# Performance work log

Measured on AMD Instinct MI355X. Metric: run time of the kernel, lower is better.

Reference implementation:

```python
import jax, jax.numpy as jnp
import numpy as np

NC, NU, K, C, P, O = 20, 16, 128, 2048, 5, 256

def setup_inputs() -> dict:
    key = jax.random.key(0)
    ks = jax.random.split(key, 6)
    s = 0.02  # keep activations well-scaled
    return {
        "topk_feats": jax.random.normal(ks[0], (NC, NU, K, C), jnp.float32),
        "prototypes": jax.random.normal(ks[1], (NC, P, C), jnp.float32),
        "w_inner1": jax.random.normal(ks[2], (O, C), jnp.float32) * s,
        "w_inner_trans": jax.random.normal(ks[3], (C, C), jnp.float32) * s,
        "w_inter1": jax.random.normal(ks[4], (O, C), jnp.float32) * s,
        "w_inter2": jax.random.normal(ks[5], (O, C), jnp.float32) * s,
    }

def reference(topk_feats, prototypes, w_inner1, w_inner_trans, w_inter1, w_inter2):
    scale = 1.0 / jnp.sqrt(jnp.asarray(O, topk_feats.dtype))
    # --- inner (per-group) self-attention, vmapped over (class, unlabel) ---
    # fe: [nc, nu, k, o]
    fe = jnp.einsum("nukc,oc->nuko", topk_feats, w_inner1)
    att = jax.nn.softmax(jnp.einsum("nuko,nulo->nukl", fe, fe) * scale, axis=-1)
    agg = jnp.einsum("nukl,nulc->nukc", att, topk_feats)  # atte @ feat
    feats = topk_feats + jax.nn.relu(jnp.einsum("nukc,dc->nukd", agg, w_inner_trans))
    # --- inter (prototype -> all feats) cross-attention per class ---
    fa = feats.reshape(NC, NU * K, C)  # cat over unlabel dim
    fae = jnp.einsum("nmc,oc->nmo", fa, w_inter1)
    pe = jnp.einsum("npc,oc->npo", prototypes, w_inter2)
    att2 = jax.nn.softmax(jnp.einsum("npo,nmo->npm", pe, fae) * scale, axis=-1)
    un_protos = jnp.einsum("npm,nmc->npc", att2, fa)  # [nc, p, c]
    return un_protos
```

## Files before the change

kernel.cpp:

```cpp
#include <hip/hip_runtime.h>

typedef __attribute__((ext_vector_type(4))) float f32x4;
typedef __attribute__((ext_vector_type(8))) short short8;

#define DEVI static __device__ __forceinline__

DEVI unsigned short f2bf(float f) {
  unsigned int u = __float_as_uint(f);
  u += 0x7FFFu + ((u >> 16) & 1u);
  return (unsigned short)(u >> 16);
}
DEVI float bf2f(unsigned short s) { return __uint_as_float(((unsigned int)s) << 16); }
DEVI unsigned int pack2(float lo, float hi) {
  return ((unsigned int)f2bf(hi) << 16) | (unsigned int)f2bf(lo);
}

#define GL2LDS(gp, lp)                                                        \
  __builtin_amdgcn_global_load_lds(                                           \
      (const __attribute__((address_space(1))) void*)(const void*)(gp),       \
      (__attribute__((address_space(3))) void*)(void*)(lp), 16, 0, 0)

#define BARRIER __builtin_amdgcn_s_barrier()
#define LGKM0                                                                 \
  do {                                                                        \
    asm volatile("s_waitcnt lgkmcnt(0)" ::: "memory");                        \
    __builtin_amdgcn_sched_barrier(0);                                        \
  } while (0)

__global__ __launch_bounds__(256) void k_cvt_bf16(const float* __restrict__ src,
                                                  unsigned short* __restrict__ dst, int n4) {
  int i = blockIdx.x * 256 + threadIdx.x;
  if (i < n4) {
    float4 v = ((const float4*)src)[i];
    uint2 o; o.x = pack2(v.x, v.y); o.y = pack2(v.z, v.w);
    ((uint2*)dst)[i] = o;
  }
}

template <bool RES>
__global__ __launch_bounds__(256) void k_gemm_bt(const unsigned short* __restrict__ A,
                                                 const unsigned short* __restrict__ B,
                                                 unsigned short* __restrict__ C,
                                                 const float* __restrict__ resid, int N) {
  constexpr int K = 2048;
  __shared__ unsigned short lA[2][128 * 64];
  __shared__ unsigned short lB[2][128 * 64];
  const int tid = threadIdx.x;
  const int lane = tid & 63;
  const int wave = tid >> 6;
  const int wr = wave >> 1, wc = wave & 1;
  const int nx = gridDim.x;
  const int lin = blockIdx.y * nx + blockIdx.x;
  const int cpx = (nx * gridDim.y) >> 3;
  const int swz = (lin & 7) * cpx + (lin >> 3);
  const long mBase = (long)(swz / nx) * 128;
  const long nBase = (long)(swz % nx) * 128;

  f32x4 acc[4][4] = {};

  auto stage = [&](int buf, int k0) {
#pragma unroll
    for (int it = 0; it < 4; it++) {
      int idx = it * 256 + tid;
      int row = idx >> 3, kc = idx & 7;
      int skc = kc ^ (row & 7);
      int lbase = (it * 256 + (tid & ~63)) * 8;
      GL2LDS(A + (mBase + row) * (long)K + k0 + skc * 8, &lA[buf][lbase]);
      GL2LDS(B + (nBase + row) * (long)K + k0 + skc * 8, &lB[buf][lbase]);
    }
  };

  stage(0, 0);
  for (int t = 0; t < 32; t++) {
    const int cur = t & 1;
    if (t < 31) {
      stage(cur ^ 1, (t + 1) * 64);
      asm volatile("s_waitcnt vmcnt(8)" ::: "memory");
    } else {
      asm volatile("s_waitcnt vmcnt(0)" ::: "memory");
    }
    __builtin_amdgcn_s_barrier();
    __builtin_amdgcn_sched_barrier(0);
    const unsigned short* bA = &lA[cur][0];
    const unsigned short* bB = &lB[cur][0];
#pragma unroll
    for (int kb = 0; kb < 2; kb++) {
      short8 af[4], bfr[4];
#pragma unroll
      for (int mt = 0; mt < 4; mt++) {
        int row = wr * 64 + mt * 16 + (lane & 15);
        int slot = (kb * 4 + (lane >> 4)) ^ (row & 7);
        af[mt] = *(const short8*)&bA[row * 64 + slot * 8];
      }
#pragma unroll
      for (int nt = 0; nt < 4; nt++) {
        int row = wc * 64 + nt * 16 + (lane & 15);
        int slot = (kb * 4 + (lane >> 4)) ^ (row & 7);
        bfr[nt] = *(const short8*)&bB[row * 64 + slot * 8];
      }
#pragma unroll
      for (int mt = 0; mt < 4; mt++)
#pragma unroll
        for (int nt = 0; nt < 4; nt++)
          acc[mt][nt] = __builtin_amdgcn_mfma_f32_16x16x32_bf16(af[mt], bfr[nt], acc[mt][nt], 0, 0, 0);
    }
    __builtin_amdgcn_sched_barrier(0);
    __builtin_amdgcn_s_barrier();
  }
#pragma unroll
  for (int mt = 0; mt < 4; mt++) {
#pragma unroll
    for (int nt = 0; nt < 4; nt++) {
#pragma unroll
      for (int j = 0; j < 4; j++) {
        long row = mBase + wr * 64 + mt * 16 + (lane >> 4) * 4 + j;
        long col = nBase + wc * 64 + nt * 16 + (lane & 15);
        float v = acc[mt][nt][j];
        if constexpr (RES) v = resid[row * (long)N + col] + fmaxf(v, 0.0f);
        C[row * (long)N + col] = f2bf(v);
      }
    }
  }
}

template <bool RES>
__global__ __launch_bounds__(512, 1) void k_gemm256_8p(const unsigned short* __restrict__ A,
                                                       const unsigned short* __restrict__ B,
                                                       unsigned short* __restrict__ C,
                                                       const unsigned short* __restrict__ residb,
                                                       int N) {
  constexpr int K = 2048;
  __shared__ unsigned short lA[2][2][128 * 64];
  __shared__ unsigned short lB[2][2][128 * 64];
  const int tid = threadIdx.x;
  const int lane = tid & 63;
  const int wave = tid >> 6;
  const int wr = wave >> 2, wc = wave & 3;
  const int lin = blockIdx.y * 8 + blockIdx.x;
  const int swz = (lin & 7) * 160 + (lin >> 3);
  const long mBase = (long)(swz >> 3) * 256;
  const long nBase = (long)(swz & 7) * 256;

  f32x4 acc[8][4] = {};
  short8 af[4][2];
  short8 bfr[4][2];

  auto stageA = [&](int buf, int half, int t) {
    const unsigned short* base = A + (mBase + half * 128) * (long)K + (long)t * 64;
    unsigned short* lds = &lA[buf][half][0];
#pragma unroll
    for (int it = 0; it < 2; it++) {
      int r = it * 64 + (tid >> 3);
      int kc = tid & 7;
      int skc = kc ^ (r & 7);
      GL2LDS(base + (long)r * K + skc * 8, lds + (it * 512 + (tid & ~63)) * 8);
    }
  };
  auto stageB = [&](int buf, int half, int t) {
    const unsigned short* base = B + (nBase + half * 128) * (long)K + (long)t * 64;
    unsigned short* lds = &lB[buf][half][0];
#pragma unroll
    for (int it = 0; it < 2; it++) {
      int r = it * 64 + (tid >> 3);
      int kc = tid & 7;
      int skc = kc ^ (r & 7);
      GL2LDS(base + (long)r * K + skc * 8, lds + (it * 512 + (tid & ~63)) * 8);
    }
  };
  auto readA = [&](int buf, int mhalf) {
#pragma unroll
    for (int mt = 0; mt < 4; mt++)
#pragma unroll
      for (int kb = 0; kb < 2; kb++) {
        int r = mhalf * 64 + mt * 16 + (lane & 15);
        int slot = (kb * 4 + (lane >> 4)) ^ (r & 7);
        af[mt][kb] = *(const short8*)&lA[buf][wr][r * 64 + slot * 8];
      }
  };
  auto readB = [&](int buf, int nh) {
#pragma unroll
    for (int ntl = 0; ntl < 2; ntl++)
#pragma unroll
      for (int kb = 0; kb < 2; kb++) {
        int nt = nh * 2 + ntl;
        int col = wc * 64 + nt * 16 + (lane & 15);
        int half = col >> 7, r = col & 127;
        int slot = (kb * 4 + (lane >> 4)) ^ (r & 7);
        bfr[nt][kb] = *(const short8*)&lB[buf][half][r * 64 + slot * 8];
      }
  };
  auto mfmaQ = [&](int mhalf, int nh) {
    __builtin_amdgcn_s_setprio(1);
#pragma unroll
    for (int kb = 0; kb < 2; kb++)
#pragma unroll
      for (int mt = 0; mt < 4; mt++)
#pragma unroll
        for (int ntl = 0; ntl < 2; ntl++) {
          int nt = nh * 2 + ntl;
          acc[mhalf * 4 + mt][nt] = __builtin_amdgcn_mfma_f32_16x16x32_bf16(
              af[mt][kb], bfr[nt][kb], acc[mhalf * 4 + mt][nt], 0, 0, 0);
        }
    __builtin_amdgcn_s_setprio(0);
  };

  stageA(0, 0, 0); stageA(0, 1, 0); stageB(0, 0, 0); stageB(0, 1, 0);
  stageA(1, 0, 1); stageA(1, 1, 1); stageB(1, 0, 1); stageB(1, 1, 1);
  asm volatile("s_waitcnt vmcnt(8)" ::: "memory");
  BARRIER;

  for (int t = 0; t < 32; t++) {
    const int cur = t & 1;
    readA(cur, 0);
    readB(cur, 0);
    if (t >= 1 && t <= 30) stageA(cur ^ 1, 1, t + 1);
    BARRIER; LGKM0;
    mfmaQ(0, 0);
    BARRIER;
    readB(cur, 1);
    BARRIER; LGKM0;
    mfmaQ(0, 1);
    BARRIER;
    readA(cur, 1);
    if (t <= 29) stageB(cur, 0, t + 2);
    BARRIER; LGKM0;
    mfmaQ(1, 0);
    BARRIER;
    if (t <= 29) { stageB(cur, 1, t + 2); stageA(cur, 0, t + 2); }
    mfmaQ(1, 1);
    if (t <= 29) {
      asm volatile("s_waitcnt vmcnt(6)" ::: "memory");
    } else if (t == 30) {
      asm volatile("s_waitcnt vmcnt(0)" ::: "memory");
    }
    BARRIER;
  }

#pragma unroll
  for (int mt = 0; mt < 8; mt++) {
#pragma unroll
    for (int nt = 0; nt < 4; nt++) {
#pragma unroll
      for (int j = 0; j < 4; j++) {
        long row = mBase + wr * 128 + mt * 16 + (lane >> 4) * 4 + j;
        long col = nBase + wc * 64 + nt * 16 + (lane & 15);
        float v = acc[mt][nt][j];
        if constexpr (RES) v = bf2f(residb[row * (long)N + col]) + fmaxf(v, 0.0f);
        C[row * (long)N + col] = f2bf(v);
      }
    }
  }
}

__global__ __launch_bounds__(256) void k_attn_inner(const unsigned short* __restrict__ fe,
                                                    const unsigned short* __restrict__ topkb,
                                                    unsigned short* __restrict__ agg) {
  __shared__ unsigned short attb[128 * 136];
  __shared__ unsigned short featT[64 * 128];
  __shared__ float redmax[2 * 128];
  __shared__ float redsum[2 * 128];
  const int tid = threadIdx.x;
  const int lane = tid & 63;
  const int wave = tid >> 6;
  const int wr = wave >> 1, wc = wave & 1;
  const int g = blockIdx.x;
  const unsigned short* feG = fe + (long)g * 128 * 256;

  f32x4 s[4][4] = {};
#pragma unroll
  for (int kb = 0; kb < 8; kb++) {
    short8 af[4], bfr[4];
#pragma unroll
    for (int mt = 0; mt < 4; mt++) {
      int row = wr * 64 + mt * 16 + (lane & 15);
      af[mt] = *(const short8*)(feG + row * 256 + kb * 32 + (lane >> 4) * 8);
    }
#pragma unroll
    for (int nt = 0; nt < 4; nt++) {
      int row = wc * 64 + nt * 16 + (lane & 15);
      bfr[nt] = *(const short8*)(feG + row * 256 + kb * 32 + (lane >> 4) * 8);
    }
#pragma unroll
    for (int mt = 0; mt < 4; mt++)
#pragma unroll
      for (int nt = 0; nt < 4; nt++)
        s[mt][nt] = __builtin_amdgcn_mfma_f32_16x16x32_bf16(af[mt], bfr[nt], s[mt][nt], 0, 0, 0);
  }

  const float cexp = 0.0625f * 1.44269504088896f;
#pragma unroll
  for (int mt = 0; mt < 4; mt++) {
#pragma unroll
    for (int j = 0; j < 4; j++) {
      float m = fmaxf(fmaxf(s[mt][0][j], s[mt][1][j]), fmaxf(s[mt][2][j], s[mt][3][j]));
#pragma unroll
      for (int d = 1; d < 16; d <<= 1) m = fmaxf(m, __shfl_xor(m, d, 64));
      int r = wr * 64 + mt * 16 + (lane >> 4) * 4 + j;
      if ((lane & 15) == 0) redmax[wc * 128 + r] = m;
    }
  }
  __syncthreads();
#pragma unroll
  for (int mt = 0; mt < 4; mt++) {
#pragma unroll
    for (int j = 0; j < 4; j++) {
      int r = wr * 64 + mt * 16 + (lane >> 4) * 4 + j;
      float M = fmaxf(redmax[r], redmax[128 + r]);
      float sm = 0.f;
#pragma unroll
      for (int nt = 0; nt < 4; nt++) {
        float p = exp2f((s[mt][nt][j] - M) * cexp);
        s[mt][nt][j] = p;
        sm += p;
      }
#pragma unroll
      for (int d = 1; d < 16; d <<= 1) sm += __shfl_xor(sm, d, 64);
      if ((lane & 15) == 0) redsum[wc * 128 + r] = sm;
    }
  }
  __syncthreads();
#pragma unroll
  for (int mt = 0; mt < 4; mt++) {
#pragma unroll
    for (int j = 0; j < 4; j++) {
      int r = wr * 64 + mt * 16 + (lane >> 4) * 4 + j;
      float inv = 1.0f / (redsum[r] + redsum[128 + r]);
#pragma unroll
      for (int nt = 0; nt < 4; nt++) {
        int c = wc * 64 + nt * 16 + (lane & 15);
        attb[r * 136 + c] = f2bf(s[mt][nt][j] * inv);
      }
    }
  }

  for (int ch = 0; ch < 32; ch++) {
    __syncthreads();
#pragma unroll
    for (int i = 0; i < 4; i++) {
      int seg = i * 256 + tid;
      int l = seg >> 3, kc = seg & 7;
      const unsigned short* gp = topkb + ((long)g * 128 + l) * 2048 + ch * 64 + kc * 8;
      uint4 w = *(const uint4*)gp;
      unsigned short v[8];
      v[0] = (unsigned short)(w.x & 0xffff); v[1] = (unsigned short)(w.x >> 16);
      v[2] = (unsigned short)(w.y & 0xffff); v[3] = (unsigned short)(w.y >> 16);
      v[4] = (unsigned short)(w.z & 0xffff); v[5] = (unsigned short)(w.z >> 16);
      v[6] = (unsigned short)(w.w & 0xffff); v[7] = (unsigned short)(w.w >> 16);
      int lx = l ^ (kc << 3);
#pragma unroll
      for (int j = 0; j < 8; j++) featT[(kc * 8 + j) * 128 + lx] = v[j];
    }
    __syncthreads();
    f32x4 c[2][4] = {};
#pragma unroll
    for (int kb = 0; kb < 4; kb++) {
      short8 af2[2], bf2v[4];
#pragma unroll
      for (int mt = 0; mt < 2; mt++) {
        int r = wave * 32 + mt * 16 + (lane & 15);
        af2[mt] = *(const short8*)&attb[r * 136 + kb * 32 + (lane >> 4) * 8];
      }
#pragma unroll
      for (int nt = 0; nt < 4; nt++) {
        int cc = nt * 16 + (lane & 15);
        int l0 = (kb * 32 + (lane >> 4) * 8) ^ (((cc >> 3) & 7) << 3);
        bf2v[nt] = *(const short8*)&featT[cc * 128 + l0];
      }
#pragma unroll
      for (int mt = 0; mt < 2; mt++)
#pragma unroll
        for (int nt = 0; nt < 4; nt++)
          c[mt][nt] = __builtin_amdgcn_mfma_f32_16x16x32_bf16(af2[mt], bf2v[nt], c[mt][nt], 0, 0, 0);
    }
#pragma unroll
    for (int mt = 0; mt < 2; mt++)
#pragma unroll
      for (int nt = 0; nt < 4; nt++)
#pragma unroll
        for (int j = 0; j < 4; j++) {
          long row = (long)g * 128 + wave * 32 + mt * 16 + (lane >> 4) * 4 + j;
          int col = ch * 64 + nt * 16 + (lane & 15);
          agg[row * 2048 + col] = f2bf(c[mt][nt][j]);
        }
  }
}

__global__ __launch_bounds__(256) void k_pe(const float* __restrict__ protos,
                                            const float* __restrict__ wi2,
                                            float* __restrict__ pe) {
  int n = blockIdx.x, oc = blockIdx.y, tid = threadIdx.x;
  if (tid < 160) {
    int p = tid >> 5, o = oc * 32 + (tid & 31);
    const float* pr = protos + ((long)n * 5 + p) * 2048;
    const float* wr = wi2 + (long)o * 2048;
    float acc = 0.f;
    for (int cidx = 0; cidx < 2048; cidx += 4) {
      float4 a = *(const float4*)(pr + cidx);
      float4 b = *(const float4*)(wr + cidx);
      acc += a.x * b.x + a.y * b.y + a.z * b.z + a.w * b.w;
    }
    pe[((long)n * 5 + p) * 256 + o] = acc;
  }
}

__global__ __launch_bounds__(256) void k_q(const float* __restrict__ pe,
                                           const float* __restrict__ wi1,
                                           float* __restrict__ q) {
  __shared__ float pel[1280];
  int n = blockIdx.x, cb = blockIdx.y, tid = threadIdx.x;
  for (int i = tid; i < 1280; i += 256) pel[i] = pe[(long)n * 1280 + i];
  __syncthreads();
  int c = cb * 256 + tid;
  float a[5] = {0.f, 0.f, 0.f, 0.f, 0.f};
  for (int o = 0; o < 256; o++) {
    float w = wi1[(long)o * 2048 + c];
#pragma unroll
    for (int p = 0; p < 5; p++) a[p] += pel[p * 256 + o] * w;
  }
#pragma unroll
  for (int p = 0; p < 5; p++) q[((long)n * 5 + p) * 2048 + c] = a[p];
}

__global__ __launch_bounds__(256) void k_lg(const float* __restrict__ q,
                                            const unsigned short* __restrict__ feats,
                                            float* __restrict__ lgp) {
  __shared__ float ql[5 * 1024];
  int n = blockIdx.x, mc = blockIdx.y, cb = blockIdx.z, tid = threadIdx.x;
  const float4* qs = (const float4*)(q + (long)n * 5 * 2048);
  for (int i = tid; i < 1280; i += 256) {
    int p = i >> 8, r = i & 255;
    ((float4*)ql)[i] = qs[p * 512 + cb * 256 + r];
  }
  __syncthreads();
  int m = mc * 256 + tid;
  const unsigned short* fr = feats + ((long)n * 2048 + m) * 2048 + cb * 1024;
  float a[5] = {0.f, 0.f, 0.f, 0.f, 0.f};
  for (int c = 0; c < 1024; c += 8) {
    uint4 w = *(const uint4*)(fr + c);
    float f[8];
    f[0] = bf2f((unsigned short)(w.x & 0xffff)); f[1] = bf2f((unsigned short)(w.x >> 16));
    f[2] = bf2f((unsigned short)(w.y & 0xffff)); f[3] = bf2f((unsigned short)(w.y >> 16));
    f[4] = bf2f((unsigned short)(w.z & 0xffff)); f[5] = bf2f((unsigned short)(w.z >> 16));
    f[6] = bf2f((unsigned short)(w.w & 0xffff)); f[7] = bf2f((unsigned short)(w.w >> 16));
#pragma unroll
    for (int j = 0; j < 8; j++) {
      float fv = f[j];
#pragma unroll
      for (int p = 0; p < 5; p++) a[p] += fv * ql[p * 1024 + c + j];
    }
  }
#pragma unroll
  for (int p = 0; p < 5; p++)
    lgp[((long)cb * 100 + n * 5 + p) * 2048 + m] = a[p] * 0.0625f;
}

__global__ __launch_bounds__(256) void k_sm(const float* __restrict__ lgp,
                                            float* __restrict__ att2) {
  __shared__ float red[4], red2[4];
  int b = blockIdx.x, tid = threadIdx.x;
  const float* s0 = lgp + (long)b * 2048;
  const float* s1 = lgp + (long)100 * 2048 + (long)b * 2048;
  float v[8];
  float mx = -1e30f;
#pragma unroll
  for (int i = 0; i < 8; i++) {
    v[i] = s0[i * 256 + tid] + s1[i * 256 + tid];
    mx = fmaxf(mx, v[i]);
  }
#pragma unroll
  for (int d = 1; d < 64; d <<= 1) mx = fmaxf(mx, __shfl_xor(mx, d, 64));
  if ((tid & 63) == 0) red[tid >> 6] = mx;
  __syncthreads();
  mx = fmaxf(fmaxf(red[0], red[1]), fmaxf(red[2], red[3]));
  float sm = 0.f;
#pragma unroll
  for (int i = 0; i < 8; i++) { v[i] = exp2f((v[i] - mx) * 1.44269504088896f); sm += v[i]; }
#pragma unroll
  for (int d = 1; d < 64; d <<= 1) sm += __shfl_xor(sm, d, 64);
  if ((tid & 63) == 0) red2[tid >> 6] = sm;
  __syncthreads();
  float inv = 1.0f / (red2[0] + red2[1] + red2[2] + red2[3]);
  float* dst = att2 + (long)b * 2048;
#pragma unroll
  for (int i = 0; i < 8; i++) dst[i * 256 + tid] = v[i] * inv;
}

__global__ __launch_bounds__(256) void k_out_part(const float* __restrict__ att2,
                                                  const unsigned short* __restrict__ feats,
                                                  float* __restrict__ partial) {
  __shared__ float a2[5 * 512];
  int n = blockIdx.x, cb = blockIdx.y, ms = blockIdx.z;
  int tid = threadIdx.x;
  const float* src = att2 + (long)n * 5 * 2048 + ms * 512;
  for (int i = tid; i < 640; i += 256) {
    int p = i >> 7, qq = i & 127;
    ((float4*)a2)[i] = *(const float4*)(src + p * 2048 + qq * 4);
  }
  __syncthreads();
  int c0 = cb * 512 + tid * 2;
  const unsigned short* fp = feats + ((long)n * 2048 + ms * 512) * 2048 + c0;
  float acc[5][2] = {};
  for (int m = 0; m < 512; m++) {
    unsigned int w = *(const unsigned int*)(fp + (long)m * 2048);
    float f0 = bf2f((unsigned short)(w & 0xffff));
    float f1 = bf2f((unsigned short)(w >> 16));
#pragma unroll
    for (int p = 0; p < 5; p++) {
      float a = a2[p * 512 + m];
      acc[p][0] += a * f0;
      acc[p][1] += a * f1;
    }
  }
  float* pp = partial + ((long)ms * 100 + (long)n * 5) * 2048;
#pragma unroll
  for (int p = 0; p < 5; p++) {
    float2 o; o.x = acc[p][0]; o.y = acc[p][1];
    *(float2*)(pp + p * 2048 + c0) = o;
  }
}

__global__ __launch_bounds__(256) void k_out_red(const float* __restrict__ partial,
                                                 float* __restrict__ outp) {
  int i = blockIdx.x * 256 + threadIdx.x;
  const f32x4* P = (const f32x4*)partial;
  f32x4 s = P[i] + P[51200 + i] + P[2 * 51200 + i] + P[3 * 51200 + i];
  ((f32x4*)outp)[i] = s;
}

extern "C" void kernel_launch(void* const* d_in, const int* in_sizes, int n_in,
                              void* d_out, int out_size, void* d_ws, size_t ws_size,
                              hipStream_t stream) {
  const float* topk = (const float*)d_in[0];
  const float* protos = (const float*)d_in[1];
  const float* w1 = (const float*)d_in[2];
  const float* wt = (const float*)d_in[3];
  const float* wi1 = (const float*)d_in[4];
  const float* wi2 = (const float*)d_in[5];
  float* outp = (float*)d_out;

  char* ws = (char*)d_ws;
  size_t off = 0;
  auto alloc = [&](size_t bytes) -> void* {
    void* p = ws + off;
    off += (bytes + 255) & ~(size_t)255;
    return p;
  };
  unsigned short* w1b = (unsigned short*)alloc((size_t)256 * 2048 * 2);
  unsigned short* wtb = (unsigned short*)alloc((size_t)2048 * 2048 * 2);
  unsigned short* topkb = (unsigned short*)alloc((size_t)40960 * 2048 * 2);
  unsigned short* fe = (unsigned short*)alloc((size_t)40960 * 256 * 2);
  unsigned short* agg = (unsigned short*)alloc((size_t)40960 * 2048 * 2);
  float* pe = (float*)alloc((size_t)20 * 5 * 256 * 4);
  float* q = (float*)alloc((size_t)20 * 5 * 2048 * 4);
  float* lgp = (float*)alloc((size_t)2 * 100 * 2048 * 4);
  float* att2 = (float*)alloc((size_t)20 * 5 * 2048 * 4);
  float* partial = (float*)alloc((size_t)4 * 100 * 2048 * 4);
  unsigned short* feats = topkb;

  k_cvt_bf16<<<512, 256, 0, stream>>>(w1, w1b, 131072);
  k_cvt_bf16<<<4096, 256, 0, stream>>>(wt, wtb, 1048576);
  k_cvt_bf16<<<81920, 256, 0, stream>>>(topk, topkb, 20971520);

  k_gemm_bt<false><<<dim3(2, 320), 256, 0, stream>>>(topkb, w1b, fe, nullptr, 256);
  k_attn_inner<<<320, 256, 0, stream>>>(fe, topkb, agg);
  k_gemm256_8p<true><<<dim3(8, 160), 512, 0, stream>>>(agg, wtb, feats, topkb, 2048);
  k_pe<<<dim3(20, 8), 256, 0, stream>>>(protos, wi2, pe);
  k_q<<<dim3(20, 8), 256, 0, stream>>>(pe, wi1, q);
  k_lg<<<dim3(20, 8, 2), 256, 0, stream>>>(q, feats, lgp);
  k_sm<<<100, 256, 0, stream>>>(lgp, att2);
  k_out_part<<<dim3(20, 4, 4), 256, 0, stream>>>(att2, feats, partial);
  k_out_red<<<200, 256, 0, stream>>>(partial, outp);
}
```

Measured before the change: 898.8 us.

## Fuse topk fp32-to-bf16 conversion into the fe GEMM and split inter-attention kernels wider

The fp32 top-k features are now read directly by a new fe GEMM kernel. It converts them to bf16 in registers, writes the bf16 copy to global memory for later stages, and feeds them to MFMA through LDS. The w1 operand is loaded straight from global into registers. This removes the separate large conversion pass and one re-read of the bf16 features. The k_lg and k_out_part kernels split the reduction over 8 chunks instead of 2 or 4, which raises grid parallelism at the cost of more partial buffers to reduce.

```diff
diff --git a/kernel.cpp b/kernel.cpp
--- a/kernel.cpp
+++ b/kernel.cpp
@@ -37,90 +37,104 @@
   }
 }
 
-template <bool RES>
-__global__ __launch_bounds__(256) void k_gemm_bt(const unsigned short* __restrict__ A,
-                                                 const unsigned short* __restrict__ B,
-                                                 unsigned short* __restrict__ C,
-                                                 const float* __restrict__ resid, int N) {
-  constexpr int K = 2048;
-  __shared__ unsigned short lA[2][128 * 64];
-  __shared__ unsigned short lB[2][128 * 64];
+__global__ __launch_bounds__(512, 1) void k_fe(const float* __restrict__ topk,
+                                               const unsigned short* __restrict__ w1b,
+                                               unsigned short* __restrict__ topkb,
+                                               unsigned short* __restrict__ fe) {
+  __shared__ unsigned short lA[128 * 64];
   const int tid = threadIdx.x;
   const int lane = tid & 63;
   const int wave = tid >> 6;
-  const int wr = wave >> 1, wc = wave & 1;
-  const int nx = gridDim.x;
-  const int lin = blockIdx.y * nx + blockIdx.x;
-  const int cpx = (nx * gridDim.y) >> 3;
-  const int swz = (lin & 7) * cpx + (lin >> 3);
-  const long mBase = (long)(swz / nx) * 128;
-  const long nBase = (long)(swz % nx) * 128;
+  const int wr = wave >> 2, wc = wave & 3;
+  const long mBase = (long)blockIdx.x * 128;
+
+  const int arow = tid >> 2;
+  const int aq = tid & 3;
+  const float* aptr = topk + (mBase + arow) * 2048 + aq * 16;
 
   f32x4 acc[4][4] = {};
-
-  auto stage = [&](int buf, int k0) {
-#pragma unroll
-    for (int it = 0; it < 4; it++) {
-      int idx = it * 256 + tid;
-      int row = idx >> 3, kc = idx & 7;
-      int skc = kc ^ (row & 7);
-      int lbase = (it * 256 + (tid & ~63)) * 8;
-      GL2LDS(A + (mBase + row) * (long)K + k0 + skc * 8, &lA[buf][lbase]);
-      GL2LDS(B + (nBase + row) * (long)K + k0 + skc * 8, &lB[buf][lbase]);
-    }
-  };
-
-  stage(0, 0);
+  float4 a4[2][4];
+  short8 bfv[2][4][2];
+
+  auto loadB = [&](int buf, int t) {
+#pragma unroll
+    for (int nt = 0; nt < 4; nt++)
+#pragma unroll
+      for (int kb = 0; kb < 2; kb++) {
+        int o = wc * 64 + nt * 16 + (lane & 15);
+        bfv[buf][nt][kb] =
+            *(const short8*)(w1b + (long)o * 2048 + t * 64 + kb * 32 + (lane >> 4) * 8);
+      }
+  };
+  auto loadA = [&](int buf, int t) {
+#pragma unroll
+    for (int i = 0; i < 4; i++) a4[buf][i] = *(const float4*)(aptr + t * 64 + i * 4);
+  };
+
+  loadB(0, 0);
+  loadA(0, 0);
+
   for (int t = 0; t < 32; t++) {
     const int cur = t & 1;
     if (t < 31) {
-      stage(cur ^ 1, (t + 1) * 64);
-      asm volatile("s_waitcnt vmcnt(8)" ::: "memory");
+      loadB(cur ^ 1, t + 1);
+      loadA(cur ^ 1, t + 1);
+      asm volatile("s_waitcnt vmcnt(12)" ::: "memory");
     } else {
       asm volatile("s_waitcnt vmcnt(0)" ::: "memory");
     }
-    __builtin_amdgcn_s_barrier();
     __builtin_amdgcn_sched_barrier(0);
-    const unsigned short* bA = &lA[cur][0];
-    const unsigned short* bB = &lB[cur][0];
-#pragma unroll
-    for (int kb = 0; kb < 2; kb++) {
-      short8 af[4], bfr[4];
-#pragma unroll
-      for (int mt = 0; mt < 4; mt++) {
-        int row = wr * 64 + mt * 16 + (lane & 15);
-        int slot = (kb * 4 + (lane >> 4)) ^ (row & 7);
-        af[mt] = *(const short8*)&bA[row * 64 + slot * 8];
-      }
-#pragma unroll
-      for (int nt = 0; nt < 4; nt++) {
-        int row = wc * 64 + nt * 16 + (lane & 15);
-        int slot = (kb * 4 + (lane >> 4)) ^ (row & 7);
-        bfr[nt] = *(const short8*)&bB[row * 64 + slot * 8];
-      }
+    unsigned int u[8];
+#pragma unroll
+    for (int i = 0; i < 4; i++) {
+      u[2 * i] = pack2(a4[cur][i].x, a4[cur][i].y);
+      u[2 * i + 1] = pack2(a4[cur][i].z, a4[cur][i].w);
+    }
+    uint4 w0 = make_uint4(u[0], u[1], u[2], u[3]);
+    uint4 w1v = make_uint4(u[4], u[5], u[6], u[7]);
+    {
+      unsigned short* dst = topkb + (mBase + arow) * 2048 + t * 64 + aq * 16;
+      *(uint4*)dst = w0;
+      *(uint4*)(dst + 8) = w1v;
+      int s0 = (aq * 2) ^ (arow & 7);
+      int s1 = (aq * 2 + 1) ^ (arow & 7);
+      *(uint4*)&lA[arow * 64 + s0 * 8] = w0;
+      *(uint4*)&lA[arow * 64 + s1 * 8] = w1v;
+    }
+    asm volatile("s_waitcnt lgkmcnt(0)" ::: "memory");
+    BARRIER;
+    short8 af[4][2];
+#pragma unroll
+    for (int mt = 0; mt < 4; mt++)
+#pragma unroll
+      for (int kb = 0; kb < 2; kb++) {
+        int r = wr * 64 + mt * 16 + (lane & 15);
+        int slot = (kb * 4 + (lane >> 4)) ^ (r & 7);
+        af[mt][kb] = *(const short8*)&lA[r * 64 + slot * 8];
+      }
+    LGKM0;
+    __builtin_amdgcn_s_setprio(1);
+#pragma unroll
+    for (int kb = 0; kb < 2; kb++)
 #pragma unroll
       for (int mt = 0; mt < 4; mt++)
 #pragma unroll
         for (int nt = 0; nt < 4; nt++)
-          acc[mt][nt] = __builtin_amdgcn_mfma_f32_16x16x32_bf16(af[mt], bfr[nt], acc[mt][nt], 0, 0, 0);
-    }
-    __builtin_amdgcn_sched_barrier(0);
-    __builtin_amdgcn_s_barrier();
-  }
-#pragma unroll
-  for (int mt = 0; mt < 4; mt++) {
-#pragma unroll
-    for (int nt = 0; nt < 4; nt++) {
+          acc[mt][nt] = __builtin_amdgcn_mfma_f32_16x16x32_bf16(af[mt][kb], bfv[cur][nt][kb],
+                                                                acc[mt][nt], 0, 0, 0);
+    __builtin_amdgcn_s_setprio(0);
+    BARRIER;
+  }
+#pragma unroll
+  for (int mt = 0; mt < 4; mt++)
+#pragma unroll
+    for (int nt = 0; nt < 4; nt++)
 #pragma unroll
       for (int j = 0; j < 4; j++) {
         long row = mBase + wr * 64 + mt * 16 + (lane >> 4) * 4 + j;
-        long col = nBase + wc * 64 + nt * 16 + (lane & 15);
-        float v = acc[mt][nt][j];
-        if constexpr (RES) v = resid[row * (long)N + col] + fmaxf(v, 0.0f);
-        C[row * (long)N + col] = f2bf(v);
-      }
-    }
-  }
+        int col = wc * 64 + nt * 16 + (lane & 15);
+        fe[row * 256 + col] = f2bf(acc[mt][nt][j]);
+      }
 }
 
 template <bool RES>
@@ -424,18 +438,18 @@
 __global__ __launch_bounds__(256) void k_lg(const float* __restrict__ q,
                                             const unsigned short* __restrict__ feats,
                                             float* __restrict__ lgp) {
-  __shared__ float ql[5 * 1024];
+  __shared__ float ql[5 * 256];
   int n = blockIdx.x, mc = blockIdx.y, cb = blockIdx.z, tid = threadIdx.x;
   const float4* qs = (const float4*)(q + (long)n * 5 * 2048);
-  for (int i = tid; i < 1280; i += 256) {
-    int p = i >> 8, r = i & 255;
-    ((float4*)ql)[i] = qs[p * 512 + cb * 256 + r];
+  for (int i = tid; i < 320; i += 256) {
+    int p = i >> 6, r = i & 63;
+    ((float4*)ql)[i] = qs[p * 512 + cb * 64 + r];
   }
   __syncthreads();
   int m = mc * 256 + tid;
-  const unsigned short* fr = feats + ((long)n * 2048 + m) * 2048 + cb * 1024;
+  const unsigned short* fr = feats + ((long)n * 2048 + m) * 2048 + cb * 256;
   float a[5] = {0.f, 0.f, 0.f, 0.f, 0.f};
-  for (int c = 0; c < 1024; c += 8) {
+  for (int c = 0; c < 256; c += 8) {
     uint4 w = *(const uint4*)(fr + c);
     float f[8];
     f[0] = bf2f((unsigned short)(w.x & 0xffff)); f[1] = bf2f((unsigned short)(w.x >> 16));
@@ -446,7 +460,7 @@
     for (int j = 0; j < 8; j++) {
       float fv = f[j];
 #pragma unroll
-      for (int p = 0; p < 5; p++) a[p] += fv * ql[p * 1024 + c + j];
+      for (int p = 0; p < 5; p++) a[p] += fv * ql[p * 256 + c + j];
     }
   }
 #pragma unroll
@@ -458,14 +472,15 @@
                                             float* __restrict__ att2) {
   __shared__ float red[4], red2[4];
   int b = blockIdx.x, tid = threadIdx.x;
-  const float* s0 = lgp + (long)b * 2048;
-  const float* s1 = lgp + (long)100 * 2048 + (long)b * 2048;
   float v[8];
   float mx = -1e30f;
 #pragma unroll
   for (int i = 0; i < 8; i++) {
-    v[i] = s0[i * 256 + tid] + s1[i * 256 + tid];
-    mx = fmaxf(mx, v[i]);
+    float s = 0.f;
+#pragma unroll
+    for (int cb = 0; cb < 8; cb++) s += lgp[(long)cb * 204800 + (long)b * 2048 + i * 256 + tid];
+    v[i] = s;
+    mx = fmaxf(mx, s);
   }
 #pragma unroll
   for (int d = 1; d < 64; d <<= 1) mx = fmaxf(mx, __shfl_xor(mx, d, 64));
@@ -488,25 +503,25 @@
 __global__ __launch_bounds__(256) void k_out_part(const float* __restrict__ att2,
                                                   const unsigned short* __restrict__ feats,
                                                   float* __restrict__ partial) {
-  __shared__ float a2[5 * 512];
+  __shared__ float a2[5 * 256];
   int n = blockIdx.x, cb = blockIdx.y, ms = blockIdx.z;
   int tid = threadIdx.x;
-  const float* src = att2 + (long)n * 5 * 2048 + ms * 512;
-  for (int i = tid; i < 640; i += 256) {
-    int p = i >> 7, qq = i & 127;
-    ((float4*)a2)[i] = *(const float4*)(src + p * 2048 + qq * 4);
+  const float* src = att2 + (long)n * 5 * 2048 + ms * 256;
+  for (int i = tid; i < 320; i += 256) {
+    int p = i >> 6, r = i & 63;
+    ((float4*)a2)[i] = *(const float4*)(src + p * 2048 + r * 4);
   }
   __syncthreads();
   int c0 = cb * 512 + tid * 2;
-  const unsigned short* fp = feats + ((long)n * 2048 + ms * 512) * 2048 + c0;
+  const unsigned short* fp = feats + ((long)n * 2048 + ms * 256) * 2048 + c0;
   float acc[5][2] = {};
-  for (int m = 0; m < 512; m++) {
+  for (int m = 0; m < 256; m++) {
     unsigned int w = *(const unsigned int*)(fp + (long)m * 2048);
     float f0 = bf2f((unsigned short)(w & 0xffff));
     float f1 = bf2f((unsigned short)(w >> 16));
 #pragma unroll
     for (int p = 0; p < 5; p++) {
-      float a = a2[p * 512 + m];
+      float a = a2[p * 256 + m];
       acc[p][0] += a * f0;
       acc[p][1] += a * f1;
     }
@@ -523,7 +538,9 @@
                                                  float* __restrict__ outp) {
   int i = blockIdx.x * 256 + threadIdx.x;
   const f32x4* P = (const f32x4*)partial;
-  f32x4 s = P[i] + P[51200 + i] + P[2 * 51200 + i] + P[3 * 51200 + i];
+  f32x4 s = P[i];
+#pragma unroll
+  for (int j = 1; j < 8; j++) s += P[(long)j * 51200 + i];
   ((f32x4*)outp)[i] = s;
 }
 
@@ -552,22 +569,21 @@
   unsigned short* agg = (unsigned short*)alloc((size_t)40960 * 2048 * 2);
   float* pe = (float*)alloc((size_t)20 * 5 * 256 * 4);
   float* q = (float*)alloc((size_t)20 * 5 * 2048 * 4);
-  float* lgp = (float*)alloc((size_t)2 * 100 * 2048 * 4);
+  float* lgp = (float*)alloc((size_t)8 * 100 * 2048 * 4);
   float* att2 = (float*)alloc((size_t)20 * 5 * 2048 * 4);
-  float* partial = (float*)alloc((size_t)4 * 100 * 2048 * 4);
+  float* partial = (float*)alloc((size_t)8 * 100 * 2048 * 4);
   unsigned short* feats = topkb;
 
   k_cvt_bf16<<<512, 256, 0, stream>>>(w1, w1b, 131072);
   k_cvt_bf16<<<4096, 256, 0, stream>>>(wt, wtb, 1048576);
-  k_cvt_bf16<<<81920, 256, 0, stream>>>(topk, topkb, 20971520);
-
-  k_gemm_bt<false><<<dim3(2, 320), 256, 0, stream>>>(topkb, w1b, fe, nullptr, 256);
+
+  k_fe<<<320, 512, 0, stream>>>(topk, w1b, topkb, fe);
   k_attn_inner<<<320, 256, 0, stream>>>(fe, topkb, agg);
   k_gemm256_8p<true><<<dim3(8, 160), 512, 0, stream>>>(agg, wtb, feats, topkb, 2048);
   k_pe<<<dim3(20, 8), 256, 0, stream>>>(protos, wi2, pe);
   k_q<<<dim3(20, 8), 256, 0, stream>>>(pe, wi1, q);
-  k_lg<<<dim3(20, 8, 2), 256, 0, stream>>>(q, feats, lgp);
+  k_lg<<<dim3(20, 8, 8), 256, 0, stream>>>(q, feats, lgp);
   k_sm<<<100, 256, 0, stream>>>(lgp, att2);
-  k_out_part<<<dim3(20, 4, 4), 256, 0, stream>>>(att2, feats, partial);
+  k_out_part<<<dim3(20, 4, 8), 256, 0, stream>>>(att2, feats, partial);
   k_out_red<<<200, 256, 0, stream>>>(partial, outp);
 }
```

Measured after the change: 1.400 ms. +55.7%, slower.

## Fuse prototype-logit dot products into trans GEMM epilogue, drop k_lg

Applied to the files above, without the earlier changes.

The big residual GEMM epilogue now computes, for each output row, partial dot products of the fresh feats with the precomputed q vectors. It reduces them across lanes and waves through shared memory and writes per-column-chunk partial logits, which k_sm then sums over 8 chunks. This removes the separate k_lg pass that re-read the whole 160 MB bf16 feats tensor, at the cost of a heavier epilogue, more LDS and 8-way partials. The k_pe and k_q launches move earlier so q is ready, the small GEMM gets a shift-based tile index, and k_out_part handles 4 columns per thread with half the blocks.

```diff
diff --git a/kernel.cpp b/kernel.cpp
--- a/kernel.cpp
+++ b/kernel.cpp
@@ -37,7 +37,7 @@
   }
 }
 
-template <bool RES>
+template <bool RES, bool N2>
 __global__ __launch_bounds__(256) void k_gemm_bt(const unsigned short* __restrict__ A,
                                                  const unsigned short* __restrict__ B,
                                                  unsigned short* __restrict__ C,
@@ -53,8 +53,14 @@
   const int lin = blockIdx.y * nx + blockIdx.x;
   const int cpx = (nx * gridDim.y) >> 3;
   const int swz = (lin & 7) * cpx + (lin >> 3);
-  const long mBase = (long)(swz / nx) * 128;
-  const long nBase = (long)(swz % nx) * 128;
+  long mBase, nBase;
+  if constexpr (N2) {
+    mBase = (long)(swz >> 1) * 128;
+    nBase = (long)(swz & 1) * 128;
+  } else {
+    mBase = (long)(swz / nx) * 128;
+    nBase = (long)(swz % nx) * 128;
+  }
 
   f32x4 acc[4][4] = {};
 
@@ -123,15 +129,16 @@
   }
 }
 
-template <bool RES>
 __global__ __launch_bounds__(512, 1) void k_gemm256_8p(const unsigned short* __restrict__ A,
                                                        const unsigned short* __restrict__ B,
                                                        unsigned short* __restrict__ C,
                                                        const unsigned short* __restrict__ residb,
-                                                       int N) {
+                                                       const float* __restrict__ qbuf,
+                                                       float* __restrict__ lgp, int N) {
   constexpr int K = 2048;
   __shared__ unsigned short lA[2][2][128 * 64];
   __shared__ unsigned short lB[2][2][128 * 64];
+  __shared__ float red[2][4][5][128];
   const int tid = threadIdx.x;
   const int lane = tid & 63;
   const int wave = tid >> 6;
@@ -236,19 +243,50 @@
     BARRIER;
   }
 
+  const int nIdx = (int)(mBase >> 11);
+  const int chunk = swz & 7;
+  float qv[4][5];
+#pragma unroll
+  for (int nt = 0; nt < 4; nt++) {
+    long col = nBase + wc * 64 + nt * 16 + (lane & 15);
+#pragma unroll
+    for (int p = 0; p < 5; p++) qv[nt][p] = qbuf[((long)nIdx * 5 + p) * 2048 + col];
+  }
 #pragma unroll
   for (int mt = 0; mt < 8; mt++) {
 #pragma unroll
-    for (int nt = 0; nt < 4; nt++) {
-#pragma unroll
-      for (int j = 0; j < 4; j++) {
-        long row = mBase + wr * 128 + mt * 16 + (lane >> 4) * 4 + j;
+    for (int j = 0; j < 4; j++) {
+      float s[5] = {0.f, 0.f, 0.f, 0.f, 0.f};
+      long row = mBase + wr * 128 + mt * 16 + (lane >> 4) * 4 + j;
+#pragma unroll
+      for (int nt = 0; nt < 4; nt++) {
         long col = nBase + wc * 64 + nt * 16 + (lane & 15);
         float v = acc[mt][nt][j];
-        if constexpr (RES) v = bf2f(residb[row * (long)N + col]) + fmaxf(v, 0.0f);
+        v = bf2f(residb[row * (long)N + col]) + fmaxf(v, 0.0f);
         C[row * (long)N + col] = f2bf(v);
-      }
-    }
+#pragma unroll
+        for (int p = 0; p < 5; p++) s[p] += v * qv[nt][p];
+      }
+#pragma unroll
+      for (int p = 0; p < 5; p++) {
+#pragma unroll
+        for (int d = 1; d < 16; d <<= 1) s[p] += __shfl_xor(s[p], d, 64);
+      }
+      if ((lane & 15) == 0) {
+        int lr = mt * 16 + (lane >> 4) * 4 + j;
+#pragma unroll
+        for (int p = 0; p < 5; p++) red[wr][wc][p][lr] = s[p];
+      }
+    }
+  }
+  __syncthreads();
+  const int mloc0 = (int)(mBase & 2047);
+  for (int idx = tid; idx < 1280; idx += 512) {
+    int wr2 = idx / 640;
+    int rem = idx - wr2 * 640;
+    int p = rem >> 7, r = rem & 127;
+    float sum = red[wr2][0][p][r] + red[wr2][1][p][r] + red[wr2][2][p][r] + red[wr2][3][p][r];
+    lgp[((long)chunk * 100 + nIdx * 5 + p) * 2048 + mloc0 + wr2 * 128 + r] = sum * 0.0625f;
   }
 }
 
@@ -421,51 +459,19 @@
   for (int p = 0; p < 5; p++) q[((long)n * 5 + p) * 2048 + c] = a[p];
 }
 
-__global__ __launch_bounds__(256) void k_lg(const float* __restrict__ q,
-                                            const unsigned short* __restrict__ feats,
-                                            float* __restrict__ lgp) {
-  __shared__ float ql[5 * 1024];
-  int n = blockIdx.x, mc = blockIdx.y, cb = blockIdx.z, tid = threadIdx.x;
-  const float4* qs = (const float4*)(q + (long)n * 5 * 2048);
-  for (int i = tid; i < 1280; i += 256) {
-    int p = i >> 8, r = i & 255;
-    ((float4*)ql)[i] = qs[p * 512 + cb * 256 + r];
-  }
-  __syncthreads();
-  int m = mc * 256 + tid;
-  const unsigned short* fr = feats + ((long)n * 2048 + m) * 2048 + cb * 1024;
-  float a[5] = {0.f, 0.f, 0.f, 0.f, 0.f};
-  for (int c = 0; c < 1024; c += 8) {
-    uint4 w = *(const uint4*)(fr + c);
-    float f[8];
-    f[0] = bf2f((unsigned short)(w.x & 0xffff)); f[1] = bf2f((unsigned short)(w.x >> 16));
-    f[2] = bf2f((unsigned short)(w.y & 0xffff)); f[3] = bf2f((unsigned short)(w.y >> 16));
-    f[4] = bf2f((unsigned short)(w.z & 0xffff)); f[5] = bf2f((unsigned short)(w.z >> 16));
-    f[6] = bf2f((unsigned short)(w.w & 0xffff)); f[7] = bf2f((unsigned short)(w.w >> 16));
-#pragma unroll
-    for (int j = 0; j < 8; j++) {
-      float fv = f[j];
-#pragma unroll
-      for (int p = 0; p < 5; p++) a[p] += fv * ql[p * 1024 + c + j];
-    }
-  }
-#pragma unroll
-  for (int p = 0; p < 5; p++)
-    lgp[((long)cb * 100 + n * 5 + p) * 2048 + m] = a[p] * 0.0625f;
-}
-
 __global__ __launch_bounds__(256) void k_sm(const float* __restrict__ lgp,
                                             float* __restrict__ att2) {
   __shared__ float red[4], red2[4];
   int b = blockIdx.x, tid = threadIdx.x;
-  const float* s0 = lgp + (long)b * 2048;
-  const float* s1 = lgp + (long)100 * 2048 + (long)b * 2048;
   float v[8];
   float mx = -1e30f;
 #pragma unroll
   for (int i = 0; i < 8; i++) {
-    v[i] = s0[i * 256 + tid] + s1[i * 256 + tid];
-    mx = fmaxf(mx, v[i]);
+    float s = 0.f;
+#pragma unroll
+    for (int cb = 0; cb < 8; cb++) s += lgp[(long)cb * 204800 + (long)b * 2048 + i * 256 + tid];
+    v[i] = s;
+    mx = fmaxf(mx, s);
   }
 #pragma unroll
   for (int d = 1; d < 64; d <<= 1) mx = fmaxf(mx, __shfl_xor(mx, d, 64));
@@ -497,25 +503,26 @@
     ((float4*)a2)[i] = *(const float4*)(src + p * 2048 + qq * 4);
   }
   __syncthreads();
-  int c0 = cb * 512 + tid * 2;
+  int c0 = cb * 1024 + tid * 4;
   const unsigned short* fp = feats + ((long)n * 2048 + ms * 512) * 2048 + c0;
-  float acc[5][2] = {};
+  float acc[5][4] = {};
   for (int m = 0; m < 512; m++) {
-    unsigned int w = *(const unsigned int*)(fp + (long)m * 2048);
-    float f0 = bf2f((unsigned short)(w & 0xffff));
-    float f1 = bf2f((unsigned short)(w >> 16));
+    uint2 w = *(const uint2*)(fp + (long)m * 2048);
+    float f0 = bf2f((unsigned short)(w.x & 0xffff));
+    float f1 = bf2f((unsigned short)(w.x >> 16));
+    float f2 = bf2f((unsigned short)(w.y & 0xffff));
+    float f3 = bf2f((unsigned short)(w.y >> 16));
 #pragma unroll
     for (int p = 0; p < 5; p++) {
       float a = a2[p * 512 + m];
-      acc[p][0] += a * f0;
-      acc[p][1] += a * f1;
+      acc[p][0] += a * f0; acc[p][1] += a * f1; acc[p][2] += a * f2; acc[p][3] += a * f3;
     }
   }
   float* pp = partial + ((long)ms * 100 + (long)n * 5) * 2048;
 #pragma unroll
   for (int p = 0; p < 5; p++) {
-    float2 o; o.x = acc[p][0]; o.y = acc[p][1];
-    *(float2*)(pp + p * 2048 + c0) = o;
+    float4 o; o.x = acc[p][0]; o.y = acc[p][1]; o.z = acc[p][2]; o.w = acc[p][3];
+    *(float4*)(pp + p * 2048 + c0) = o;
   }
 }
 
@@ -552,7 +559,7 @@
   unsigned short* agg = (unsigned short*)alloc((size_t)40960 * 2048 * 2);
   float* pe = (float*)alloc((size_t)20 * 5 * 256 * 4);
   float* q = (float*)alloc((size_t)20 * 5 * 2048 * 4);
-  float* lgp = (float*)alloc((size_t)2 * 100 * 2048 * 4);
+  float* lgp = (float*)alloc((size_t)8 * 100 * 2048 * 4);
   float* att2 = (float*)alloc((size_t)20 * 5 * 2048 * 4);
   float* partial = (float*)alloc((size_t)4 * 100 * 2048 * 4);
   unsigned short* feats = topkb;
@@ -560,14 +567,13 @@
   k_cvt_bf16<<<512, 256, 0, stream>>>(w1, w1b, 131072);
   k_cvt_bf16<<<4096, 256, 0, stream>>>(wt, wtb, 1048576);
   k_cvt_bf16<<<81920, 256, 0, stream>>>(topk, topkb, 20971520);
-
-  k_gemm_bt<false><<<dim3(2, 320), 256, 0, stream>>>(topkb, w1b, fe, nullptr, 256);
-  k_attn_inner<<<320, 256, 0, stream>>>(fe, topkb, agg);
-  k_gemm256_8p<true><<<dim3(8, 160), 512, 0, stream>>>(agg, wtb, feats, topkb, 2048);
   k_pe<<<dim3(20, 8), 256, 0, stream>>>(protos, wi2, pe);
   k_q<<<dim3(20, 8), 256, 0, stream>>>(pe, wi1, q);
-  k_lg<<<dim3(20, 8, 2), 256, 0, stream>>>(q, feats, lgp);
+
+  k_gemm_bt<false, true><<<dim3(2, 320), 256, 0, stream>>>(topkb, w1b, fe, nullptr, 256);
+  k_attn_inner<<<320, 256, 0, stream>>>(fe, topkb, agg);
+  k_gemm256_8p<<<dim3(8, 160), 512, 0, stream>>>(agg, wtb, feats, topkb, q, lgp, 2048);
   k_sm<<<100, 256, 0, stream>>>(lgp, att2);
-  k_out_part<<<dim3(20, 4, 4), 256, 0, stream>>>(att2, feats, partial);
+  k_out_part<<<dim3(20, 2, 4), 256, 0, stream>>>(att2, feats, partial);
   k_out_red<<<200, 256, 0, stream>>>(partial, outp);
 }
```

After: 959.2 us. 6.7% more time.

## Split B fragments and prefetch next-tile B reads in the 256x256 GEMM; retile output kernel

Applied to the files above, without the earlier changes.

The main 256x256 GEMM now keeps B fragments in two register sets (columns 0-1 and 2-3), reads the next tile's first B half at the end of each iteration, and restages A with different vmcnt waits, so LDS reads overlap MFMA work. The projection GEMM gets a compile-time path that replaces division and modulo with shifts when there are two N tiles. The final weighted-sum kernel processes 4 columns per thread with 8 m-splits, and the reduction sums 8 partials. The prototype projection kernels are moved earlier in the launch order. The new waitcnt schedule adds a risk of ordering or race errors.

```diff
diff --git a/kernel.cpp b/kernel.cpp
--- a/kernel.cpp
+++ b/kernel.cpp
@@ -37,7 +37,7 @@
   }
 }
 
-template <bool RES>
+template <bool RES, bool N2>
 __global__ __launch_bounds__(256) void k_gemm_bt(const unsigned short* __restrict__ A,
                                                  const unsigned short* __restrict__ B,
                                                  unsigned short* __restrict__ C,
@@ -53,8 +53,14 @@
   const int lin = blockIdx.y * nx + blockIdx.x;
   const int cpx = (nx * gridDim.y) >> 3;
   const int swz = (lin & 7) * cpx + (lin >> 3);
-  const long mBase = (long)(swz / nx) * 128;
-  const long nBase = (long)(swz % nx) * 128;
+  long mBase, nBase;
+  if constexpr (N2) {
+    mBase = (long)(swz >> 1) * 128;
+    nBase = (long)(swz & 1) * 128;
+  } else {
+    mBase = (long)(swz / nx) * 128;
+    nBase = (long)(swz % nx) * 128;
+  }
 
   f32x4 acc[4][4] = {};
 
@@ -143,7 +149,8 @@
 
   f32x4 acc[8][4] = {};
   short8 af[4][2];
-  short8 bfr[4][2];
+  short8 b01[2][2];
+  short8 b23[2][2];
 
   auto stageA = [&](int buf, int half, int t) {
     const unsigned short* base = A + (mBase + half * 128) * (long)K + (long)t * 64;
@@ -177,57 +184,79 @@
         af[mt][kb] = *(const short8*)&lA[buf][wr][r * 64 + slot * 8];
       }
   };
-  auto readB = [&](int buf, int nh) {
+  auto readB01 = [&](int buf) {
 #pragma unroll
     for (int ntl = 0; ntl < 2; ntl++)
 #pragma unroll
       for (int kb = 0; kb < 2; kb++) {
-        int nt = nh * 2 + ntl;
-        int col = wc * 64 + nt * 16 + (lane & 15);
+        int col = wc * 64 + ntl * 16 + (lane & 15);
         int half = col >> 7, r = col & 127;
         int slot = (kb * 4 + (lane >> 4)) ^ (r & 7);
-        bfr[nt][kb] = *(const short8*)&lB[buf][half][r * 64 + slot * 8];
-      }
-  };
-  auto mfmaQ = [&](int mhalf, int nh) {
+        b01[ntl][kb] = *(const short8*)&lB[buf][half][r * 64 + slot * 8];
+      }
+  };
+  auto readB23 = [&](int buf) {
+#pragma unroll
+    for (int ntl = 0; ntl < 2; ntl++)
+#pragma unroll
+      for (int kb = 0; kb < 2; kb++) {
+        int col = wc * 64 + (2 + ntl) * 16 + (lane & 15);
+        int half = col >> 7, r = col & 127;
+        int slot = (kb * 4 + (lane >> 4)) ^ (r & 7);
+        b23[ntl][kb] = *(const short8*)&lB[buf][half][r * 64 + slot * 8];
+      }
+  };
+  auto mfmaQ01 = [&](int mh) {
     __builtin_amdgcn_s_setprio(1);
 #pragma unroll
     for (int kb = 0; kb < 2; kb++)
 #pragma unroll
       for (int mt = 0; mt < 4; mt++)
 #pragma unroll
-        for (int ntl = 0; ntl < 2; ntl++) {
-          int nt = nh * 2 + ntl;
-          acc[mhalf * 4 + mt][nt] = __builtin_amdgcn_mfma_f32_16x16x32_bf16(
-              af[mt][kb], bfr[nt][kb], acc[mhalf * 4 + mt][nt], 0, 0, 0);
-        }
+        for (int ntl = 0; ntl < 2; ntl++)
+          acc[mh * 4 + mt][ntl] = __builtin_amdgcn_mfma_f32_16x16x32_bf16(
+              af[mt][kb], b01[ntl][kb], acc[mh * 4 + mt][ntl], 0, 0, 0);
     __builtin_amdgcn_s_setprio(0);
   };
+  auto mfmaQ23 = [&](int mh) {
+    __builtin_amdgcn_s_setprio(1);
+#pragma unroll
+    for (int kb = 0; kb < 2; kb++)
+#pragma unroll
+      for (int mt = 0; mt < 4; mt++)
+#pragma unroll
+        for (int ntl = 0; ntl < 2; ntl++)
+          acc[mh * 4 + mt][2 + ntl] = __builtin_amdgcn_mfma_f32_16x16x32_bf16(
+              af[mt][kb], b23[ntl][kb], acc[mh * 4 + mt][2 + ntl], 0, 0, 0);
+    __builtin_amdgcn_s_setprio(0);
+  };
 
   stageA(0, 0, 0); stageA(0, 1, 0); stageB(0, 0, 0); stageB(0, 1, 0);
-  stageA(1, 0, 1); stageA(1, 1, 1); stageB(1, 0, 1); stageB(1, 1, 1);
-  asm volatile("s_waitcnt vmcnt(8)" ::: "memory");
+  stageB(1, 0, 1); stageB(1, 1, 1); stageA(1, 0, 1);
+  asm volatile("s_waitcnt vmcnt(6)" ::: "memory");
   BARRIER;
+  readB01(0);
 
   for (int t = 0; t < 32; t++) {
     const int cur = t & 1;
     readA(cur, 0);
-    readB(cur, 0);
-    if (t >= 1 && t <= 30) stageA(cur ^ 1, 1, t + 1);
+    if (t <= 30) stageA(cur ^ 1, 1, t + 1);
     BARRIER; LGKM0;
-    mfmaQ(0, 0);
+    mfmaQ01(0);
     BARRIER;
-    readB(cur, 1);
+    readB23(cur);
     BARRIER; LGKM0;
-    mfmaQ(0, 1);
+    mfmaQ23(0);
     BARRIER;
     readA(cur, 1);
     if (t <= 29) stageB(cur, 0, t + 2);
+    if (t <= 30) asm volatile("s_waitcnt vmcnt(4)" ::: "memory");
     BARRIER; LGKM0;
-    mfmaQ(1, 0);
+    mfmaQ01(1);
     BARRIER;
     if (t <= 29) { stageB(cur, 1, t + 2); stageA(cur, 0, t + 2); }
-    mfmaQ(1, 1);
+    mfmaQ23(1);
+    if (t <= 30) readB01(cur ^ 1);
     if (t <= 29) {
       asm volatile("s_waitcnt vmcnt(6)" ::: "memory");
     } else if (t == 30) {
@@ -488,34 +517,35 @@
 __global__ __launch_bounds__(256) void k_out_part(const float* __restrict__ att2,
                                                   const unsigned short* __restrict__ feats,
                                                   float* __restrict__ partial) {
-  __shared__ float a2[5 * 512];
+  __shared__ float a2[5 * 256];
   int n = blockIdx.x, cb = blockIdx.y, ms = blockIdx.z;
   int tid = threadIdx.x;
-  const float* src = att2 + (long)n * 5 * 2048 + ms * 512;
-  for (int i = tid; i < 640; i += 256) {
-    int p = i >> 7, qq = i & 127;
-    ((float4*)a2)[i] = *(const float4*)(src + p * 2048 + qq * 4);
+  const float* src = att2 + (long)n * 5 * 2048 + ms * 256;
+  for (int i = tid; i < 320; i += 256) {
+    int p = i >> 6, r = i & 63;
+    ((float4*)a2)[i] = *(const float4*)(src + p * 2048 + r * 4);
   }
   __syncthreads();
-  int c0 = cb * 512 + tid * 2;
-  const unsigned short* fp = feats + ((long)n * 2048 + ms * 512) * 2048 + c0;
-  float acc[5][2] = {};
-  for (int m = 0; m < 512; m++) {
-    unsigned int w = *(const unsigned int*)(fp + (long)m * 2048);
-    float f0 = bf2f((unsigned short)(w & 0xffff));
-    float f1 = bf2f((unsigned short)(w >> 16));
+  int c0 = cb * 1024 + tid * 4;
+  const unsigned short* fp = feats + ((long)n * 2048 + ms * 256) * 2048 + c0;
+  float acc[5][4] = {};
+  for (int m = 0; m < 256; m++) {
+    uint2 w = *(const uint2*)(fp + (long)m * 2048);
+    float f0 = bf2f((unsigned short)(w.x & 0xffff));
+    float f1 = bf2f((unsigned short)(w.x >> 16));
+    float f2 = bf2f((unsigned short)(w.y & 0xffff));
+    float f3 = bf2f((unsigned short)(w.y >> 16));
 #pragma unroll
     for (int p = 0; p < 5; p++) {
-      float a = a2[p * 512 + m];
-      acc[p][0] += a * f0;
-      acc[p][1] += a * f1;
+      float a = a2[p * 256 + m];
+      acc[p][0] += a * f0; acc[p][1] += a * f1; acc[p][2] += a * f2; acc[p][3] += a * f3;
     }
   }
   float* pp = partial + ((long)ms * 100 + (long)n * 5) * 2048;
 #pragma unroll
   for (int p = 0; p < 5; p++) {
-    float2 o; o.x = acc[p][0]; o.y = acc[p][1];
-    *(float2*)(pp + p * 2048 + c0) = o;
+    float4 o; o.x = acc[p][0]; o.y = acc[p][1]; o.z = acc[p][2]; o.w = acc[p][3];
+    *(float4*)(pp + p * 2048 + c0) = o;
   }
 }
 
@@ -523,7 +553,9 @@
                                                  float* __restrict__ outp) {
   int i = blockIdx.x * 256 + threadIdx.x;
   const f32x4* P = (const f32x4*)partial;
-  f32x4 s = P[i] + P[51200 + i] + P[2 * 51200 + i] + P[3 * 51200 + i];
+  f32x4 s = P[i];
+#pragma unroll
+  for (int j = 1; j < 8; j++) s += P[(long)j * 51200 + i];
   ((f32x4*)outp)[i] = s;
 }
 
@@ -554,20 +586,20 @@
   float* q = (float*)alloc((size_t)20 * 5 * 2048 * 4);
   float* lgp = (float*)alloc((size_t)2 * 100 * 2048 * 4);
   float* att2 = (float*)alloc((size_t)20 * 5 * 2048 * 4);
-  float* partial = (float*)alloc((size_t)4 * 100 * 2048 * 4);
+  float* partial = (float*)alloc((size_t)8 * 100 * 2048 * 4);
   unsigned short* feats = topkb;
 
   k_cvt_bf16<<<512, 256, 0, stream>>>(w1, w1b, 131072);
   k_cvt_bf16<<<4096, 256, 0, stream>>>(wt, wtb, 1048576);
   k_cvt_bf16<<<81920, 256, 0, stream>>>(topk, topkb, 20971520);
-
-  k_gemm_bt<false><<<dim3(2, 320), 256, 0, stream>>>(topkb, w1b, fe, nullptr, 256);
+  k_pe<<<dim3(20, 8), 256, 0, stream>>>(protos, wi2, pe);
+  k_q<<<dim3(20, 8), 256, 0, stream>>>(pe, wi1, q);
+
+  k_gemm_bt<false, true><<<dim3(2, 320), 256, 0, stream>>>(topkb, w1b, fe, nullptr, 256);
   k_attn_inner<<<320, 256, 0, stream>>>(fe, topkb, agg);
   k_gemm256_8p<true><<<dim3(8, 160), 512, 0, stream>>>(agg, wtb, feats, topkb, 2048);
-  k_pe<<<dim3(20, 8), 256, 0, stream>>>(protos, wi2, pe);
-  k_q<<<dim3(20, 8), 256, 0, stream>>>(pe, wi1, q);
   k_lg<<<dim3(20, 8, 2), 256, 0, stream>>>(q, feats, lgp);
   k_sm<<<100, 256, 0, stream>>>(lgp, att2);
-  k_out_part<<<dim3(20, 4, 4), 256, 0, stream>>>(att2, feats, partial);
+  k_out_part<<<dim3(20, 2, 8), 256, 0, stream>>>(att2, feats, partial);
   k_out_red<<<200, 256, 0, stream>>>(partial, outp);
 }
```

Result: slower. 945.4 us (+5.2%).
